# Optimization experiments

Hardware: AMD Instinct MI355X
Metric: run time of the kernel (lower is better)

The kernel has to match this reference:

```python
import jax, jax.numpy as jnp
import numpy as np

B = 65536
H = W = 28
K = 3
OUT_HW = H - K + 1  # 26, valid conv
FEAT = OUT_HW * OUT_HW  # 676
HID = 200
NCLS = 10


def setup_inputs() -> dict:
    key = jax.random.key(0)
    ks = jax.random.split(key, 6)
    x = jax.random.normal(ks[0], (B, H * W), dtype=jnp.float32)
    conv_w = jnp.ones((K, K), dtype=jnp.float32)  # Parameter(ones((3,3)))
    w1 = jax.random.normal(ks[1], (FEAT, HID), dtype=jnp.float32) * (1.0 / np.sqrt(FEAT))
    b1 = jnp.zeros((HID,), dtype=jnp.float32)
    w2 = jax.random.normal(ks[2], (HID, NCLS), dtype=jnp.float32) * (1.0 / np.sqrt(HID))
    b2 = jnp.zeros((NCLS,), dtype=jnp.float32)
    return {"x": x, "conv_w": conv_w, "w1": w1, "b1": b1, "w2": w2, "b2": b2}


def _forward(x, conv_w, w1, b1, w2, b2):
    img = x.reshape(-1, H, W)  # (B,28,28)
    # valid 3x3 single-channel cross-correlation (matches input[i:i+3,j:j+3]*w)
    lhs = img[:, None, :, :]          # (B,1,28,28)
    rhs = conv_w[None, None, :, :]    # (1,1,3,3)
    conv = jax.lax.conv_general_dilated(
        lhs, rhs, window_strides=(1, 1), padding="VALID",
        dimension_numbers=("NCHW", "OIHW", "NCHW"))  # (B,1,26,26)
    feat = conv.reshape(-1, FEAT)     # (B,676)
    hidden = jax.nn.relu(feat @ w1 + b1)  # (B,200)
    return hidden @ w2 + b2               # (B,10) logits


def reference(x, conv_w, w1, b1, w2, b2):
    return _forward(x, conv_w, w1, b1, w2, b2)
```

## Files before the change

### kernel.cpp

```cpp
#include <hip/hip_runtime.h>
#include <hip/hip_bf16.h>

#define BATCH   65536
#define HW      28
#define OHW     26
#define FEAT    676
#define HID     200
#define NCLS    10
#define MT2     64
#define GBLOCKS (BATCH / MT2)
#define KC1     25

typedef __attribute__((ext_vector_type(8))) __bf16 bf16x8;
typedef __attribute__((ext_vector_type(4))) float  f32x4;

__device__ __forceinline__ unsigned int pk2(float a, float b) {
  __hip_bfloat16 ha = __float2bfloat16(a), hb = __float2bfloat16(b);
  return (unsigned int)__builtin_bit_cast(unsigned short, ha)
       | ((unsigned int)__builtin_bit_cast(unsigned short, hb) << 16);
}

__device__ __forceinline__ unsigned short* fslot(unsigned short* base, int m, int k) {
  const int kc = k >> 5;
  return base + ((kc * 64 + ((k >> 3) & 3) * 16 + (m ^ (kc & 7))) * 8) + (k & 7);
}

__global__ __launch_bounds__(256) void prep_w1e(const float* __restrict__ w1,
                                                const float* __restrict__ cwp,
                                                unsigned short* __restrict__ w1e) {
  int c = blockIdx.x * 256 + threadIdx.x;
  if (c >= KC1 * 13 * 64) return;
  int lane = c & 63, g = c >> 6;
  int kc = g / 13, nt = g - kc * 13;
  int ln = lane & 15, qd = lane >> 4;
  int n = nt * 16 + ln;
  float cw[9];
  #pragma unroll
  for (int t = 0; t < 9; ++t) cw[t] = cwp[t];
  float v[8];
  #pragma unroll
  for (int j = 0; j < 8; ++j) {
    int k = kc * 32 + qd * 8 + j;
    float s = 0.f;
    if (k < 784 && n < HID) {
      int ri = k / 28, ci = k - ri * 28;
      #pragma unroll
      for (int di = 0; di < 3; ++di) {
        int r = ri - di;
        if (r >= 0 && r < OHW) {
          #pragma unroll
          for (int dj = 0; dj < 3; ++dj) {
            int cc = ci - dj;
            if (cc >= 0 && cc < OHW) s += cw[di * 3 + dj] * w1[(r * OHW + cc) * HID + n];
          }
        }
      }
    }
    v[j] = s;
  }
  uint4 o = make_uint4(pk2(v[0], v[1]), pk2(v[2], v[3]),
                       pk2(v[4], v[5]), pk2(v[6], v[7]));
  *(uint4*)(w1e + (size_t)c * 8) = o;
}

__global__ __launch_bounds__(256) void prep_w2f(const float* __restrict__ w2,
                                                unsigned short* __restrict__ w2f) {
  int c = blockIdx.x * 256 + threadIdx.x;
  if (c >= 7 * 64) return;
  int lane = c & 63, kc = c >> 6;
  int col = lane & 15;
  float v[8];
  #pragma unroll
  for (int j = 0; j < 8; ++j) {
    int k = kc * 32 + (lane >> 4) * 8 + j;
    v[j] = (col < NCLS && k < HID) ? w2[k * NCLS + col] : 0.f;
  }
  uint4 o = make_uint4(pk2(v[0], v[1]), pk2(v[2], v[3]),
                       pk2(v[4], v[5]), pk2(v[6], v[7]));
  *(uint4*)(w2f + (size_t)c * 8) = o;
}

template<int NT0, int NT>
__device__ __forceinline__ void gemm1_body(
    const float* __restrict__ x, const unsigned short* __restrict__ w1e,
    const float* __restrict__ b1, unsigned short* aBuf ,
    unsigned short* hidA, int lane, int tid, int blk64) {
  const int ln = lane & 15, qd = lane >> 4;

  const int sc_mi  = tid >> 6;
  const int sc_qd  = (tid >> 4) & 3;
  const int sc_row = tid & 15;
  const float* xrow = x + ((size_t)blk64 + sc_mi * 16 + sc_row) * 784 + sc_qd * 8;
  const int sc_off = (sc_mi * 64 + sc_qd * 16 + sc_row) * 8;

  f32x4 acc[4][NT];
  #pragma unroll
  for (int mi = 0; mi < 4; ++mi)
    #pragma unroll
    for (int t = 0; t < NT; ++t) acc[mi][t] = (f32x4){0.f, 0.f, 0.f, 0.f};

  {
    float4 f0 = *(const float4*)(xrow);
    float4 f1 = *(const float4*)(xrow + 4);
    *(uint4*)(aBuf + sc_off) = make_uint4(pk2(f0.x, f0.y), pk2(f0.z, f0.w),
                                          pk2(f1.x, f1.y), pk2(f1.z, f1.w));
  }
  __syncthreads();

  int cur = 0;
  for (int kc = 0; kc < KC1; ++kc) {
    uint4 nx;
    const bool hav = (kc + 1 < KC1);
    if (hav) {
      if (kc + 1 == KC1 - 1 && sc_qd >= 2) {
        nx = make_uint4(0u, 0u, 0u, 0u);
      } else {
        float4 f0 = *(const float4*)(xrow + (kc + 1) * 32);
        float4 f1 = *(const float4*)(xrow + (kc + 1) * 32 + 4);
        nx = make_uint4(pk2(f0.x, f0.y), pk2(f0.z, f0.w),
                        pk2(f1.x, f1.y), pk2(f1.z, f1.w));
      }
    }
    const unsigned short* ab = aBuf + cur * 2048;
    bf16x8 a[4];
    #pragma unroll
    for (int mi = 0; mi < 4; ++mi)
      a[mi] = *(const bf16x8*)(ab + mi * 512 + lane * 8);
    #pragma unroll
    for (int t = 0; t < NT; ++t) {
      bf16x8 b = *(const bf16x8*)(w1e + ((size_t)(kc * 13 + NT0 + t) * 64 + lane) * 8);
      #pragma unroll
      for (int mi = 0; mi < 4; ++mi)
        acc[mi][t] = __builtin_amdgcn_mfma_f32_16x16x32_bf16(a[mi], b, acc[mi][t], 0, 0, 0);
    }
    if (hav) *(uint4*)(aBuf + (cur ^ 1) * 2048 + sc_off) = nx;
    __syncthreads();
    cur ^= 1;
  }

  #pragma unroll
  for (int t = 0; t < NT; ++t) {
    const int n = (NT0 + t) * 16 + ln;
    if (n < HID) {
      const float bias = b1[n];
      const int kc2 = n >> 5, qd2 = (n >> 3) & 3, j2 = n & 7, c2 = kc2 & 7;
      #pragma unroll
      for (int mi = 0; mi < 4; ++mi)
        #pragma unroll
        for (int rr = 0; rr < 4; ++rr) {
          const int m = qd * 4 + rr;
          float h = fmaxf(acc[mi][t][rr] + bias, 0.f);
          __hip_bfloat16 hb = __float2bfloat16(h);
          hidA[mi * 3584 + (kc2 * 64 + qd2 * 16 + (m ^ c2)) * 8 + j2] =
              __builtin_bit_cast(unsigned short, hb);
        }
    }
  }
}

__global__ __launch_bounds__(256, 4) void fused4(
    const float* __restrict__ x, const unsigned short* __restrict__ w1e,
    const unsigned short* __restrict__ w2f, const float* __restrict__ b1,
    const float* __restrict__ b2, float* __restrict__ out) {
  __shared__ __align__(16) unsigned short aBuf[2 * 4 * 64 * 8];
  __shared__ __align__(16) unsigned short hidA[4 * 7 * 64 * 8];
  const int tid  = threadIdx.x;
  const int wave = tid >> 6;
  const int lane = tid & 63;
  const int blk64 = blockIdx.x * MT2;

  for (int i = tid; i < 768; i += 256) {
    int mi = i / 192, r = i - mi * 192, m = r / 12, d = r - m * 12;
    *(unsigned int*)fslot(hidA + mi * 3584, m, 200 + 2 * d) = 0u;
  }

  switch (wave) {
    case 0:  gemm1_body<0, 4>(x, w1e, b1, aBuf, hidA, lane, tid, blk64); break;
    case 1:  gemm1_body<4, 3>(x, w1e, b1, aBuf, hidA, lane, tid, blk64); break;
    case 2:  gemm1_body<7, 3>(x, w1e, b1, aBuf, hidA, lane, tid, blk64); break;
    default: gemm1_body<10, 3>(x, w1e, b1, aBuf, hidA, lane, tid, blk64); break;
  }
  __syncthreads();

  const int ln = lane & 15, qd = lane >> 4;
  f32x4 acc2 = (f32x4){0.f, 0.f, 0.f, 0.f};
  #pragma unroll
  for (int kc = 0; kc < 7; ++kc) {
    bf16x8 a = *(const bf16x8*)&hidA[wave * 3584 + (kc * 64 + (lane ^ (kc & 7))) * 8];
    bf16x8 b = *(const bf16x8*)(w2f + ((size_t)kc * 64 + lane) * 8);
    acc2 = __builtin_amdgcn_mfma_f32_16x16x32_bf16(a, b, acc2, 0, 0, 0);
  }
  if (ln < NCLS) {
    const float bb = b2[ln];
    #pragma unroll
    for (int rr = 0; rr < 4; ++rr) {
      out[((size_t)(blockIdx.x * 4 + wave) * 16 + qd * 4 + rr) * NCLS + ln] = acc2[rr] + bb;
    }
  }
}

extern "C" void kernel_launch(void* const* d_in, const int* in_sizes, int n_in,
                              void* d_out, int out_size, void* d_ws, size_t ws_size,
                              hipStream_t stream) {
  const float* x  = (const float*)d_in[0];
  const float* cw = (const float*)d_in[1];
  const float* w1 = (const float*)d_in[2];
  const float* b1 = (const float*)d_in[3];
  const float* w2 = (const float*)d_in[4];
  const float* b2 = (const float*)d_in[5];
  float* out = (float*)d_out;

  unsigned short* w1e = (unsigned short*)d_ws;
  unsigned short* w2f = (unsigned short*)((char*)d_ws + 335872);

  hipLaunchKernelGGL(prep_w1e, dim3((KC1 * 13 * 64 + 255) / 256), dim3(256), 0, stream,
                     w1, cw, w1e);
  hipLaunchKernelGGL(prep_w2f, dim3(2), dim3(256), 0, stream, w2, w2f);
  hipLaunchKernelGGL(fused4, dim3(GBLOCKS), dim3(256), 0, stream,
                     x, w1e, w2f, b1, b2, out);
}
```

Baseline: 323.7 us.

## Load input directly into MFMA registers instead of staging through LDS

Each wave now reads its A-operand rows of x straight from global memory, converts them to bf16 in registers and feeds them to the MFMAs. This removes the double-buffered LDS staging and the per-chunk block barrier. The cost is that each of the four waves reads the full 64-row input tile, quadrupling global/cache read traffic for x. The fully unrolled k loop also adds register pressure.

```diff
diff --git a/kernel.cpp b/kernel.cpp
--- a/kernel.cpp
+++ b/kernel.cpp
@@ -81,61 +81,43 @@
 }
 
 template<int NT0, int NT>
-__device__ __forceinline__ void gemm1_body(
+__device__ __forceinline__ void gemm1_direct(
     const float* __restrict__ x, const unsigned short* __restrict__ w1e,
-    const float* __restrict__ b1, unsigned short* aBuf ,
-    unsigned short* hidA, int lane, int tid, int blk64) {
+    const float* __restrict__ b1, unsigned short* hidA, int lane, int blk64) {
   const int ln = lane & 15, qd = lane >> 4;
 
-  const int sc_mi  = tid >> 6;
-  const int sc_qd  = (tid >> 4) & 3;
-  const int sc_row = tid & 15;
-  const float* xrow = x + ((size_t)blk64 + sc_mi * 16 + sc_row) * 784 + sc_qd * 8;
-  const int sc_off = (sc_mi * 64 + sc_qd * 16 + sc_row) * 8;
-
   f32x4 acc[4][NT];
   #pragma unroll
   for (int mi = 0; mi < 4; ++mi)
     #pragma unroll
     for (int t = 0; t < NT; ++t) acc[mi][t] = (f32x4){0.f, 0.f, 0.f, 0.f};
 
-  {
-    float4 f0 = *(const float4*)(xrow);
-    float4 f1 = *(const float4*)(xrow + 4);
-    *(uint4*)(aBuf + sc_off) = make_uint4(pk2(f0.x, f0.y), pk2(f0.z, f0.w),
-                                          pk2(f1.x, f1.y), pk2(f1.z, f1.w));
-  }
-  __syncthreads();
-
-  int cur = 0;
+  const float* xa[4];
+  #pragma unroll
+  for (int mi = 0; mi < 4; ++mi)
+    xa[mi] = x + ((size_t)(blk64 + mi * 16 + ln)) * 784 + qd * 8;
+
+  #pragma unroll
   for (int kc = 0; kc < KC1; ++kc) {
-    uint4 nx;
-    const bool hav = (kc + 1 < KC1);
-    if (hav) {
-      if (kc + 1 == KC1 - 1 && sc_qd >= 2) {
-        nx = make_uint4(0u, 0u, 0u, 0u);
+    bf16x8 b[NT];
+    #pragma unroll
+    for (int t = 0; t < NT; ++t)
+      b[t] = *(const bf16x8*)(w1e + ((size_t)(kc * 13 + NT0 + t) * 64 + lane) * 8);
+    #pragma unroll
+    for (int mi = 0; mi < 4; ++mi) {
+      union { uint4 u; bf16x8 h; } cv;
+      if (kc == KC1 - 1 && qd >= 2) {
+        cv.u = make_uint4(0u, 0u, 0u, 0u);
       } else {
-        float4 f0 = *(const float4*)(xrow + (kc + 1) * 32);
-        float4 f1 = *(const float4*)(xrow + (kc + 1) * 32 + 4);
-        nx = make_uint4(pk2(f0.x, f0.y), pk2(f0.z, f0.w),
-                        pk2(f1.x, f1.y), pk2(f1.z, f1.w));
+        const float4 f0 = *(const float4*)(xa[mi] + kc * 32);
+        const float4 f1 = *(const float4*)(xa[mi] + kc * 32 + 4);
+        cv.u = make_uint4(pk2(f0.x, f0.y), pk2(f0.z, f0.w),
+                          pk2(f1.x, f1.y), pk2(f1.z, f1.w));
       }
-    }
-    const unsigned short* ab = aBuf + cur * 2048;
-    bf16x8 a[4];
-    #pragma unroll
-    for (int mi = 0; mi < 4; ++mi)
-      a[mi] = *(const bf16x8*)(ab + mi * 512 + lane * 8);
-    #pragma unroll
-    for (int t = 0; t < NT; ++t) {
-      bf16x8 b = *(const bf16x8*)(w1e + ((size_t)(kc * 13 + NT0 + t) * 64 + lane) * 8);
       #pragma unroll
-      for (int mi = 0; mi < 4; ++mi)
-        acc[mi][t] = __builtin_amdgcn_mfma_f32_16x16x32_bf16(a[mi], b, acc[mi][t], 0, 0, 0);
-    }
-    if (hav) *(uint4*)(aBuf + (cur ^ 1) * 2048 + sc_off) = nx;
-    __syncthreads();
-    cur ^= 1;
+      for (int t = 0; t < NT; ++t)
+        acc[mi][t] = __builtin_amdgcn_mfma_f32_16x16x32_bf16(cv.h, b[t], acc[mi][t], 0, 0, 0);
+    }
   }
 
   #pragma unroll
@@ -158,11 +140,10 @@
   }
 }
 
-__global__ __launch_bounds__(256, 4) void fused4(
+__global__ __launch_bounds__(256, 4) void fused5(
     const float* __restrict__ x, const unsigned short* __restrict__ w1e,
     const unsigned short* __restrict__ w2f, const float* __restrict__ b1,
     const float* __restrict__ b2, float* __restrict__ out) {
-  __shared__ __align__(16) unsigned short aBuf[2 * 4 * 64 * 8];
   __shared__ __align__(16) unsigned short hidA[4 * 7 * 64 * 8];
   const int tid  = threadIdx.x;
   const int wave = tid >> 6;
@@ -175,10 +156,10 @@
   }
 
   switch (wave) {
-    case 0:  gemm1_body<0, 4>(x, w1e, b1, aBuf, hidA, lane, tid, blk64); break;
-    case 1:  gemm1_body<4, 3>(x, w1e, b1, aBuf, hidA, lane, tid, blk64); break;
-    case 2:  gemm1_body<7, 3>(x, w1e, b1, aBuf, hidA, lane, tid, blk64); break;
-    default: gemm1_body<10, 3>(x, w1e, b1, aBuf, hidA, lane, tid, blk64); break;
+    case 0:  gemm1_direct<0, 4>(x, w1e, b1, hidA, lane, blk64); break;
+    case 1:  gemm1_direct<4, 3>(x, w1e, b1, hidA, lane, blk64); break;
+    case 2:  gemm1_direct<7, 3>(x, w1e, b1, hidA, lane, blk64); break;
+    default: gemm1_direct<10, 3>(x, w1e, b1, hidA, lane, blk64); break;
   }
   __syncthreads();
 
@@ -216,6 +197,6 @@
   hipLaunchKernelGGL(prep_w1e, dim3((KC1 * 13 * 64 + 255) / 256), dim3(256), 0, stream,
                      w1, cw, w1e);
   hipLaunchKernelGGL(prep_w2f, dim3(2), dim3(256), 0, stream, w2, w2f);
-  hipLaunchKernelGGL(fused4, dim3(GBLOCKS), dim3(256), 0, stream,
+  hipLaunchKernelGGL(fused5, dim3(GBLOCKS), dim3(256), 0, stream,
                      x, w1e, w2f, b1, b2, out);
 }
```

After: 380.5 us. 17.6% more time.
